# Kernel tuning notes

Hardware: AMD Instinct MI355X
Metric: run time of the kernel (lower is better)

## Reference

```python
import jax, jax.numpy as jnp
import numpy as np

COLOR_SIZE = 4
SIZE = 128
LENGTH = SIZE * SIZE * 3  # 49152


def setup_inputs() -> dict:
    key = jax.random.key(0)
    k1, k2, k3, k4 = jax.random.split(key, 4)
    example = jax.random.randint(k1, (2, SIZE, SIZE, 3), 0, COLOR_SIZE, dtype=jnp.int32)
    W_in = jax.random.normal(k2, (1, 1024), dtype=jnp.float32) * 0.02
    pos_enc = jax.random.normal(k3, (LENGTH, 1024), dtype=jnp.float32)
    W_final = jax.random.normal(k4, (1024, COLOR_SIZE), dtype=jnp.float32) * 0.02
    b_final = jnp.zeros((COLOR_SIZE,), dtype=jnp.float32)
    return {"example": example, "W_in": W_in, "pos_enc": pos_enc,
            "W_final": W_final, "b_final": b_final}


def reference(example, W_in, pos_enc, W_final, b_final):
    # example: [B, 128, 128, 3] int, values in [0, color_size)
    B = example.shape[0]
    x = example.astype(jnp.float32) / COLOR_SIZE * 2.0 - 1.0
    x = x.reshape(B, LENGTH, 1)
    x = x * 2.0 - 1.0  # second scaling, as in original call()
    x = x @ W_in  # [B, L, 1] @ [1, F] -> [B, L, F]
    x = jax.nn.relu(x + pos_enc)
    # running-average via causal cumsum; factor computed in fp16 as in original
    factor = (1.0 / jnp.arange(1, LENGTH + 1, dtype=jnp.float32))
    factor = factor.astype(jnp.float16).astype(jnp.float32)[:, None]
    x = jnp.cumsum(x, axis=-2) * factor
    x = x @ W_final + b_final  # [B, L, color_size]
    x = x.reshape(B, SIZE, SIZE, 3, COLOR_SIZE)
    return x.astype(jnp.float32)
```

## Files before the change

kernel.cpp:

```cpp
#include <hip/hip_runtime.h>
#include <math.h>

#define L_TOTAL 49152
#define NBLK 768
#define ROWS_PER_BLK 64
#define NCHUNK 32

__device__ __forceinline__ float4 f4add(float4 a, float4 b) {
  return make_float4(a.x + b.x, a.y + b.y, a.z + b.z, a.w + b.w);
}

__device__ __forceinline__ float fp16_roundtrip_pos(float x) {
  unsigned u = __float_as_uint(x);
  int e = (int)((u >> 23) & 0xffu) - 127;
  unsigned m = (u & 0x7fffffu) | 0x800000u;
  int shift = (e >= -14) ? 13 : (13 + (-14 - e));
  if (shift >= 25) return 0.0f;
  unsigned keep = m >> shift;
  unsigned rem = m & ((1u << shift) - 1u);
  unsigned halfbit = 1u << (shift - 1);
  if (rem > halfbit || (rem == halfbit && (keep & 1u))) keep++;
  return ldexpf((float)keep, e + shift - 23);
}

__global__ __launch_bounds__(256, 3) void gpart_kernel(
    const int* __restrict__ ex, const float4* __restrict__ win4,
    const float4* __restrict__ pos4, const float4* __restrict__ wf4,
    float4* __restrict__ gbuf, float4* __restrict__ pp) {
  __shared__ float4 tile[2][ROWS_PER_BLK][9];
  __shared__ float4 wtot[2][4];

  const int tid = threadIdx.x;
  const int lane = tid & 63;
  const int wv = tid >> 6;
  const int rowBase = blockIdx.x * ROWS_PER_BLK;

  const int r_st = tid >> 2;
  const int q_st = tid & 3;

  const int seg = lane >> 4;
  const int r16 = lane & 15;
  const int myrow = wv * 16 + r16;
  const int grow = rowBase + myrow;

  const float s0 = (float)ex[grow] - 3.0f;
  const float s1 = (float)ex[L_TOTAL + grow] - 3.0f;

  float4 a0 = make_float4(0.f, 0.f, 0.f, 0.f);
  float4 a1 = make_float4(0.f, 0.f, 0.f, 0.f);

  const size_t prow = (size_t)(rowBase + r_st) * 256;

  tile[0][r_st][q_st]     = pos4[prow + q_st];
  tile[0][r_st][q_st + 4] = pos4[prow + q_st + 4];
  __syncthreads();

  for (int c = 0; c < NCHUNK; ++c) {
    if (c + 1 < NCHUNK) {
      const int f4n = (c + 1) * 8;
      tile[(c + 1) & 1][r_st][q_st]     = pos4[prow + f4n + q_st];
      tile[(c + 1) & 1][r_st][q_st + 4] = pos4[prow + f4n + q_st + 4];
    }
    const int f4b = c * 8 + seg * 2;
    const float4 p0 = tile[c & 1][myrow][seg * 2];
    const float4 p1 = tile[c & 1][myrow][seg * 2 + 1];
    const float4 w0 = win4[f4b];
    const float4 w1 = win4[f4b + 1];
    const float pe[8] = {p0.x, p0.y, p0.z, p0.w, p1.x, p1.y, p1.z, p1.w};
    const float we[8] = {w0.x, w0.y, w0.z, w0.w, w1.x, w1.y, w1.z, w1.w};
#pragma unroll
    for (int e = 0; e < 8; ++e) {
      const float4 wf = wf4[f4b * 4 + e];
      const float t0 = fmaxf(fmaf(s0, we[e], pe[e]), 0.0f);
      const float t1 = fmaxf(fmaf(s1, we[e], pe[e]), 0.0f);
      a0.x = fmaf(t0, wf.x, a0.x); a0.y = fmaf(t0, wf.y, a0.y);
      a0.z = fmaf(t0, wf.z, a0.z); a0.w = fmaf(t0, wf.w, a0.w);
      a1.x = fmaf(t1, wf.x, a1.x); a1.y = fmaf(t1, wf.y, a1.y);
      a1.z = fmaf(t1, wf.z, a1.z); a1.w = fmaf(t1, wf.w, a1.w);
    }
    __syncthreads();
  }

#define REDUCE8(MASK)                                                   \
  a0.x += __shfl_xor(a0.x, MASK); a0.y += __shfl_xor(a0.y, MASK);       \
  a0.z += __shfl_xor(a0.z, MASK); a0.w += __shfl_xor(a0.w, MASK);       \
  a1.x += __shfl_xor(a1.x, MASK); a1.y += __shfl_xor(a1.y, MASK);       \
  a1.z += __shfl_xor(a1.z, MASK); a1.w += __shfl_xor(a1.w, MASK);
  REDUCE8(16)
  REDUCE8(32)
#undef REDUCE8

#pragma unroll
  for (int d = 1; d < 16; d <<= 1) {
    const float u0 = __shfl_up(a0.x, d), u1 = __shfl_up(a0.y, d);
    const float u2 = __shfl_up(a0.z, d), u3 = __shfl_up(a0.w, d);
    const float u4 = __shfl_up(a1.x, d), u5 = __shfl_up(a1.y, d);
    const float u6 = __shfl_up(a1.z, d), u7 = __shfl_up(a1.w, d);
    if (r16 >= d) {
      a0.x += u0; a0.y += u1; a0.z += u2; a0.w += u3;
      a1.x += u4; a1.y += u5; a1.z += u6; a1.w += u7;
    }
  }

  float4 t0, t1;
  t0.x = __shfl(a0.x, 15); t0.y = __shfl(a0.y, 15);
  t0.z = __shfl(a0.z, 15); t0.w = __shfl(a0.w, 15);
  t1.x = __shfl(a1.x, 15); t1.y = __shfl(a1.y, 15);
  t1.z = __shfl(a1.z, 15); t1.w = __shfl(a1.w, 15);
  if (lane == 0) { wtot[0][wv] = t0; wtot[1][wv] = t1; }
  __syncthreads();
  float4 o0 = make_float4(0.f, 0.f, 0.f, 0.f);
  float4 o1 = make_float4(0.f, 0.f, 0.f, 0.f);
  for (int j = 0; j < wv; ++j) {
    o0 = f4add(o0, wtot[0][j]);
    o1 = f4add(o1, wtot[1][j]);
  }
  a0 = f4add(a0, o0);
  a1 = f4add(a1, o1);

  if (seg == 0) {
    gbuf[grow] = a0;
    gbuf[L_TOTAL + grow] = a1;
  }
  if (tid == 255) {
    pp[blockIdx.x] = a0;
    pp[NBLK + blockIdx.x] = a1;
  }
}

__global__ __launch_bounds__(128, 8) void finish_kernel(
    const float4* __restrict__ gbuf, const float4* __restrict__ pp,
    const float* __restrict__ bfin, float4* __restrict__ out4) {
  const int tid = threadIdx.x;
  const int bb = tid >> 6;
  const int i = tid & 63;
  const int bid = blockIdx.x;

  float4 q = make_float4(0.f, 0.f, 0.f, 0.f);
  for (int j = i; j < bid; j += 64) q = f4add(q, pp[bb * NBLK + j]);
#pragma unroll
  for (int off = 32; off > 0; off >>= 1) {
    q.x += __shfl_xor(q.x, off); q.y += __shfl_xor(q.y, off);
    q.z += __shfl_xor(q.z, off); q.w += __shfl_xor(q.w, off);
  }

  const int row = bid * ROWS_PER_BLK + i;
  const float4 v = f4add(gbuf[(size_t)bb * L_TOTAL + row], q);
  const float factor = fp16_roundtrip_pos(1.0f / (float)(row + 1));
  float4 o;
  o.x = fmaf(v.x, factor, bfin[0]);
  o.y = fmaf(v.y, factor, bfin[1]);
  o.z = fmaf(v.z, factor, bfin[2]);
  o.w = fmaf(v.w, factor, bfin[3]);
  out4[(size_t)bb * L_TOTAL + row] = o;
}

extern "C" void kernel_launch(void* const* d_in, const int* in_sizes, int n_in,
                              void* d_out, int out_size, void* d_ws, size_t ws_size,
                              hipStream_t stream) {
  const int* ex = (const int*)d_in[0];
  const float4* win4 = (const float4*)d_in[1];
  const float4* pos4 = (const float4*)d_in[2];
  const float4* wf4 = (const float4*)d_in[3];
  const float* bfin = (const float*)d_in[4];
  float4* out4 = (float4*)d_out;

  float4* gbuf = (float4*)d_ws;
  float4* pp = gbuf + (size_t)2 * L_TOTAL;

  gpart_kernel<<<NBLK, 256, 0, stream>>>(ex, win4, pos4, wf4, gbuf, pp);
  finish_kernel<<<NBLK, 128, 0, stream>>>(gbuf, pp, bfin, out4);
}
```

Measured before the change: 48.77 us.

## Double chunk width and prefetch pos_enc into registers two chunks ahead

New measurement: 92.76 us. 1.9x slower.

```diff
diff --git a/kernel.cpp b/kernel.cpp
--- a/kernel.cpp
+++ b/kernel.cpp
@@ -4,7 +4,7 @@
 #define L_TOTAL 49152
 #define NBLK 768
 #define ROWS_PER_BLK 64
-#define NCHUNK 32
+#define NCHUNK 16
 
 __device__ __forceinline__ float4 f4add(float4 a, float4 b) {
   return make_float4(a.x + b.x, a.y + b.y, a.z + b.z, a.w + b.w);
@@ -27,7 +27,7 @@
     const int* __restrict__ ex, const float4* __restrict__ win4,
     const float4* __restrict__ pos4, const float4* __restrict__ wf4,
     float4* __restrict__ gbuf, float4* __restrict__ pp) {
-  __shared__ float4 tile[2][ROWS_PER_BLK][9];
+  __shared__ float4 tile[2][ROWS_PER_BLK][17];
   __shared__ float4 wtot[2][4];
 
   const int tid = threadIdx.x;
@@ -51,32 +51,44 @@
 
   const size_t prow = (size_t)(rowBase + r_st) * 256;
 
-  tile[0][r_st][q_st]     = pos4[prow + q_st];
-  tile[0][r_st][q_st + 4] = pos4[prow + q_st + 4];
+  float4 st[4];
+#pragma unroll
+  for (int j = 0; j < 4; ++j)
+    tile[0][r_st][q_st + 4 * j] = pos4[prow + q_st + 4 * j];
+#pragma unroll
+  for (int j = 0; j < 4; ++j)
+    st[j] = pos4[prow + 16 + q_st + 4 * j];
   __syncthreads();
 
   for (int c = 0; c < NCHUNK; ++c) {
     if (c + 1 < NCHUNK) {
-      const int f4n = (c + 1) * 8;
-      tile[(c + 1) & 1][r_st][q_st]     = pos4[prow + f4n + q_st];
-      tile[(c + 1) & 1][r_st][q_st + 4] = pos4[prow + f4n + q_st + 4];
+#pragma unroll
+      for (int j = 0; j < 4; ++j)
+        tile[(c + 1) & 1][r_st][q_st + 4 * j] = st[j];
     }
-    const int f4b = c * 8 + seg * 2;
-    const float4 p0 = tile[c & 1][myrow][seg * 2];
-    const float4 p1 = tile[c & 1][myrow][seg * 2 + 1];
-    const float4 w0 = win4[f4b];
-    const float4 w1 = win4[f4b + 1];
-    const float pe[8] = {p0.x, p0.y, p0.z, p0.w, p1.x, p1.y, p1.z, p1.w};
-    const float we[8] = {w0.x, w0.y, w0.z, w0.w, w1.x, w1.y, w1.z, w1.w};
+    if (c + 2 < NCHUNK) {
+      const int f4n = (c + 2) * 16;
 #pragma unroll
-    for (int e = 0; e < 8; ++e) {
-      const float4 wf = wf4[f4b * 4 + e];
-      const float t0 = fmaxf(fmaf(s0, we[e], pe[e]), 0.0f);
-      const float t1 = fmaxf(fmaf(s1, we[e], pe[e]), 0.0f);
-      a0.x = fmaf(t0, wf.x, a0.x); a0.y = fmaf(t0, wf.y, a0.y);
-      a0.z = fmaf(t0, wf.z, a0.z); a0.w = fmaf(t0, wf.w, a0.w);
-      a1.x = fmaf(t1, wf.x, a1.x); a1.y = fmaf(t1, wf.y, a1.y);
-      a1.z = fmaf(t1, wf.z, a1.z); a1.w = fmaf(t1, wf.w, a1.w);
+      for (int j = 0; j < 4; ++j)
+        st[j] = pos4[prow + f4n + q_st + 4 * j];
+    }
+    const int f4b = c * 16 + seg * 4;
+#pragma unroll
+    for (int j = 0; j < 4; ++j) {
+      const float4 p = tile[c & 1][myrow][seg * 4 + j];
+      const float4 w = win4[f4b + j];
+      const float pe[4] = {p.x, p.y, p.z, p.w};
+      const float we[4] = {w.x, w.y, w.z, w.w};
+#pragma unroll
+      for (int k = 0; k < 4; ++k) {
+        const float4 wf = wf4[(f4b + j) * 4 + k];
+        const float t0 = fmaxf(fmaf(s0, we[k], pe[k]), 0.0f);
+        const float t1 = fmaxf(fmaf(s1, we[k], pe[k]), 0.0f);
+        a0.x = fmaf(t0, wf.x, a0.x); a0.y = fmaf(t0, wf.y, a0.y);
+        a0.z = fmaf(t0, wf.z, a0.z); a0.w = fmaf(t0, wf.w, a0.w);
+        a1.x = fmaf(t1, wf.x, a1.x); a1.y = fmaf(t1, wf.y, a1.y);
+        a1.z = fmaf(t1, wf.z, a1.z); a1.w = fmaf(t1, wf.w, a1.w);
+      }
     }
     __syncthreads();
   }
```

## Halve rows per block, double grid, and prefetch pos_enc through a register

Applied to the files above, without the earlier changes.

Result: slower. 51.79 us (+6.2%).

```diff
diff --git a/kernel.cpp b/kernel.cpp
--- a/kernel.cpp
+++ b/kernel.cpp
@@ -2,8 +2,8 @@
 #include <math.h>
 
 #define L_TOTAL 49152
-#define NBLK 768
-#define ROWS_PER_BLK 64
+#define NBLK 1536
+#define ROWS_PER_BLK 32
 #define NCHUNK 32
 
 __device__ __forceinline__ float4 f4add(float4 a, float4 b) {
@@ -23,7 +23,7 @@
   return ldexpf((float)keep, e + shift - 23);
 }
 
-__global__ __launch_bounds__(256, 3) void gpart_kernel(
+__global__ __launch_bounds__(256, 6) void gpart_kernel(
     const int* __restrict__ ex, const float4* __restrict__ win4,
     const float4* __restrict__ pos4, const float4* __restrict__ wf4,
     float4* __restrict__ gbuf, float4* __restrict__ pp) {
@@ -35,12 +35,12 @@
   const int wv = tid >> 6;
   const int rowBase = blockIdx.x * ROWS_PER_BLK;
 
-  const int r_st = tid >> 2;
-  const int q_st = tid & 3;
+  const int r_st = tid >> 3;
+  const int q_st = tid & 7;
 
-  const int seg = lane >> 4;
-  const int r16 = lane & 15;
-  const int myrow = wv * 16 + r16;
+  const int seg = lane >> 3;
+  const int r8 = lane & 7;
+  const int myrow = wv * 8 + r8;
   const int grow = rowBase + myrow;
 
   const float s0 = (float)ex[grow] - 3.0f;
@@ -51,28 +51,23 @@
 
   const size_t prow = (size_t)(rowBase + r_st) * 256;
 
-  tile[0][r_st][q_st]     = pos4[prow + q_st];
-  tile[0][r_st][q_st + 4] = pos4[prow + q_st + 4];
+  tile[0][r_st][q_st] = pos4[prow + q_st];
+  float4 st = pos4[prow + 8 + q_st];
   __syncthreads();
 
   for (int c = 0; c < NCHUNK; ++c) {
-    if (c + 1 < NCHUNK) {
-      const int f4n = (c + 1) * 8;
-      tile[(c + 1) & 1][r_st][q_st]     = pos4[prow + f4n + q_st];
-      tile[(c + 1) & 1][r_st][q_st + 4] = pos4[prow + f4n + q_st + 4];
-    }
-    const int f4b = c * 8 + seg * 2;
-    const float4 p0 = tile[c & 1][myrow][seg * 2];
-    const float4 p1 = tile[c & 1][myrow][seg * 2 + 1];
-    const float4 w0 = win4[f4b];
-    const float4 w1 = win4[f4b + 1];
-    const float pe[8] = {p0.x, p0.y, p0.z, p0.w, p1.x, p1.y, p1.z, p1.w};
-    const float we[8] = {w0.x, w0.y, w0.z, w0.w, w1.x, w1.y, w1.z, w1.w};
+    if (c + 1 < NCHUNK) tile[(c + 1) & 1][r_st][q_st] = st;
+    if (c + 2 < NCHUNK) st = pos4[prow + (size_t)(c + 2) * 8 + q_st];
+    const int f4i = c * 8 + seg;
+    const float4 p = tile[c & 1][myrow][seg];
+    const float4 w = win4[f4i];
+    const float pe[4] = {p.x, p.y, p.z, p.w};
+    const float we[4] = {w.x, w.y, w.z, w.w};
 #pragma unroll
-    for (int e = 0; e < 8; ++e) {
-      const float4 wf = wf4[f4b * 4 + e];
-      const float t0 = fmaxf(fmaf(s0, we[e], pe[e]), 0.0f);
-      const float t1 = fmaxf(fmaf(s1, we[e], pe[e]), 0.0f);
+    for (int k = 0; k < 4; ++k) {
+      const float4 wf = wf4[f4i * 4 + k];
+      const float t0 = fmaxf(fmaf(s0, we[k], pe[k]), 0.0f);
+      const float t1 = fmaxf(fmaf(s1, we[k], pe[k]), 0.0f);
       a0.x = fmaf(t0, wf.x, a0.x); a0.y = fmaf(t0, wf.y, a0.y);
       a0.z = fmaf(t0, wf.z, a0.z); a0.w = fmaf(t0, wf.w, a0.w);
       a1.x = fmaf(t1, wf.x, a1.x); a1.y = fmaf(t1, wf.y, a1.y);
@@ -86,27 +81,28 @@
   a0.z += __shfl_xor(a0.z, MASK); a0.w += __shfl_xor(a0.w, MASK);       \
   a1.x += __shfl_xor(a1.x, MASK); a1.y += __shfl_xor(a1.y, MASK);       \
   a1.z += __shfl_xor(a1.z, MASK); a1.w += __shfl_xor(a1.w, MASK);
+  REDUCE8(8)
   REDUCE8(16)
   REDUCE8(32)
 #undef REDUCE8
 
 #pragma unroll
-  for (int d = 1; d < 16; d <<= 1) {
+  for (int d = 1; d < 8; d <<= 1) {
     const float u0 = __shfl_up(a0.x, d), u1 = __shfl_up(a0.y, d);
     const float u2 = __shfl_up(a0.z, d), u3 = __shfl_up(a0.w, d);
     const float u4 = __shfl_up(a1.x, d), u5 = __shfl_up(a1.y, d);
     const float u6 = __shfl_up(a1.z, d), u7 = __shfl_up(a1.w, d);
-    if (r16 >= d) {
+    if (r8 >= d) {
       a0.x += u0; a0.y += u1; a0.z += u2; a0.w += u3;
       a1.x += u4; a1.y += u5; a1.z += u6; a1.w += u7;
     }
   }
 
   float4 t0, t1;
-  t0.x = __shfl(a0.x, 15); t0.y = __shfl(a0.y, 15);
-  t0.z = __shfl(a0.z, 15); t0.w = __shfl(a0.w, 15);
-  t1.x = __shfl(a1.x, 15); t1.y = __shfl(a1.y, 15);
-  t1.z = __shfl(a1.z, 15); t1.w = __shfl(a1.w, 15);
+  t0.x = __shfl(a0.x, 7); t0.y = __shfl(a0.y, 7);
+  t0.z = __shfl(a0.z, 7); t0.w = __shfl(a0.w, 7);
+  t1.x = __shfl(a1.x, 7); t1.y = __shfl(a1.y, 7);
+  t1.z = __shfl(a1.z, 7); t1.w = __shfl(a1.w, 7);
   if (lane == 0) { wtot[0][wv] = t0; wtot[1][wv] = t1; }
   __syncthreads();
   float4 o0 = make_float4(0.f, 0.f, 0.f, 0.f);
@@ -144,15 +140,17 @@
     q.z += __shfl_xor(q.z, off); q.w += __shfl_xor(q.w, off);
   }
 
-  const int row = bid * ROWS_PER_BLK + i;
-  const float4 v = f4add(gbuf[(size_t)bb * L_TOTAL + row], q);
-  const float factor = fp16_roundtrip_pos(1.0f / (float)(row + 1));
-  float4 o;
-  o.x = fmaf(v.x, factor, bfin[0]);
-  o.y = fmaf(v.y, factor, bfin[1]);
-  o.z = fmaf(v.z, factor, bfin[2]);
-  o.w = fmaf(v.w, factor, bfin[3]);
-  out4[(size_t)bb * L_TOTAL + row] = o;
+  if (i < ROWS_PER_BLK) {
+    const int row = bid * ROWS_PER_BLK + i;
+    const float4 v = f4add(gbuf[(size_t)bb * L_TOTAL + row], q);
+    const float factor = fp16_roundtrip_pos(1.0f / (float)(row + 1));
+    float4 o;
+    o.x = fmaf(v.x, factor, bfin[0]);
+    o.y = fmaf(v.y, factor, bfin[1]);
+    o.z = fmaf(v.z, factor, bfin[2]);
+    o.w = fmaf(v.w, factor, bfin[3]);
+    out4[(size_t)bb * L_TOTAL + row] = o;
+  }
 }
 
 extern "C" void kernel_launch(void* const* d_in, const int* in_sizes, int n_in,
```
